# Kernel optimization log

Hardware: AMD Instinct MI355X
Metric: run time of the kernel (lower is better)

Reference implementation:

```python
import jax, jax.numpy as jnp
import numpy as np

TAU = 0.85  # augmented=True -> tau=0.85


def _f1_rewards(labels_f):
    # labels_f: [B, L] binary relevance. Vectorized f1@(k) for k=1..L,
    # replacing the original per-element Python double loop.
    B, L = labels_f.shape
    cum = jnp.cumsum(labels_f, axis=1)                      # rel hits @ k
    k = jnp.arange(1, L + 1, dtype=labels_f.dtype)          # [L]
    prec = cum / k                                          # precision@k
    total = cum[:, -1:]                                     # total relevant per row
    rec = jnp.where(total > 0, cum / jnp.maximum(total, 1.0), 0.0)
    denom = prec + rec
    return jnp.where(denom > 0, 2.0 * prec * rec / jnp.maximum(denom, 1e-30), 0.0)


def setup_inputs() -> dict:
    key = jax.random.key(0)
    k1, k2 = jax.random.split(key)
    B, L = 1024, 4096
    raw = jax.random.uniform(k1, (B, L, 1), dtype=jnp.float32) + 1e-3
    output = raw / jnp.sum(raw, axis=1, keepdims=True)      # valid prob dist per row
    labels = jax.random.randint(k2, (B, L), 0, 2, dtype=jnp.int32)
    return {"output": output, "labels": labels}


def reference(output, labels):
    B = output.shape[0]
    r = _f1_rewards(labels.astype(jnp.float32))             # [B, L]
    q = jax.nn.softmax(r / TAU, axis=1)                     # exp(r/tau)/sum == softmax
    p = output[..., 0]                                      # squeeze(2) -> [B, L]
    logp = jnp.log(p)
    # KLDivLoss(reduction='batchmean'): sum(q * (log q - log p)) / B
    return jnp.sum(q * (jnp.log(q) - logp)) / B
```

## Files before the change

### kernel.cpp

```cpp
#include <hip/hip_runtime.h>


constexpr int L = 4096;

__global__ __launch_bounds__(256) void row_kl_kernel(const float* __restrict__ p,
                                                     const int* __restrict__ labels,
                                                     float* __restrict__ row_out) {
    const int b = blockIdx.x;
    const int t = threadIdx.x;
    const int lane = t & 63;
    const int wv = t >> 6;

    const int4* lab4 = (const int4*)(labels + (size_t)b * L) + t * 4;
    const float4* p4 = (const float4*)(p + (size_t)b * L) + t * 4;

    int4 a0 = lab4[0], a1 = lab4[1], a2 = lab4[2], a3 = lab4[3];
    float4 q0 = p4[0], q1 = p4[1], q2 = p4[2], q3 = p4[3];

    int lv[16] = {a0.x, a0.y, a0.z, a0.w, a1.x, a1.y, a1.z, a1.w,
                  a2.x, a2.y, a2.z, a2.w, a3.x, a3.y, a3.z, a3.w};
    float pv[16] = {q0.x, q0.y, q0.z, q0.w, q1.x, q1.y, q1.z, q1.w,
                    q2.x, q2.y, q2.z, q2.w, q3.x, q3.y, q3.z, q3.w};

    int tsum = 0;
    #pragma unroll
    for (int j = 0; j < 16; ++j) tsum += lv[j];

    int inc = tsum;
    #pragma unroll
    for (int d = 1; d < 64; d <<= 1) {
        int n = __shfl_up(inc, d, 64);
        if (lane >= d) inc += n;
    }

    __shared__ int wsum[4];
    __shared__ float red[8];
    if (lane == 63) wsum[wv] = inc;
    __syncthreads();
    const int w0 = wsum[0], w1 = wsum[1], w2 = wsum[2], w3 = wsum[3];
    const int T = w0 + w1 + w2 + w3;
    int run = (wv > 0 ? w0 : 0) + (wv > 1 ? w1 : 0) + (wv > 2 ? w2 : 0)
              + inc - tsum;

    const float K = 2.0f / 0.85f;
    float Zl = 0.f, Wl = 0.f;
    const int base = t * 16 + 1;
    #pragma unroll
    for (int j = 0; j < 16; ++j) {
        run += lv[j];
        float s = K * __fdividef((float)run, (float)(T + base + j));
        float e = __expf(s);
        Zl += e;
        Wl += e * (s - __logf(pv[j]));
    }

    #pragma unroll
    for (int d = 32; d >= 1; d >>= 1) {
        Zl += __shfl_down(Zl, d, 64);
        Wl += __shfl_down(Wl, d, 64);
    }
    if (lane == 0) { red[wv] = Zl; red[4 + wv] = Wl; }
    __syncthreads();
    if (t == 0) {
        float Z = red[0] + red[1] + red[2] + red[3];
        float W = red[4] + red[5] + red[6] + red[7];
        row_out[b] = W / Z - __logf(Z);
    }
}

__global__ __launch_bounds__(256) void final_reduce_kernel(const float* __restrict__ row,
                                                           float* __restrict__ out, int B) {
    const int t = threadIdx.x;
    float v = 0.f;
    for (int i = t; i < B; i += 256) v += row[i];
    #pragma unroll
    for (int d = 32; d >= 1; d >>= 1) v += __shfl_down(v, d, 64);
    __shared__ float s[4];
    if ((t & 63) == 0) s[t >> 6] = v;
    __syncthreads();
    if (t == 0) out[0] = (s[0] + s[1] + s[2] + s[3]) / (float)B;
}

extern "C" void kernel_launch(void* const* d_in, const int* in_sizes, int n_in,
                              void* d_out, int out_size, void* d_ws, size_t ws_size,
                              hipStream_t stream) {
    const float* p = (const float*)d_in[0];
    const int* labels = (const int*)d_in[1];
    const int B = in_sizes[1] / L;
    float* row = (float*)d_ws;

    row_kl_kernel<<<B, 256, 0, stream>>>(p, labels, row);
    final_reduce_kernel<<<1, 256, 0, stream>>>(row, (float*)d_out, B);
}
```

Baseline: 77.69 us.

## Coalesce row loads by interleaving per-lane chunks and scanning each chunk separately

```diff
diff --git a/kernel.cpp b/kernel.cpp
--- a/kernel.cpp
+++ b/kernel.cpp
@@ -11,47 +11,64 @@
     const int lane = t & 63;
     const int wv = t >> 6;
 
-    const int4* lab4 = (const int4*)(labels + (size_t)b * L) + t * 4;
-    const float4* p4 = (const float4*)(p + (size_t)b * L) + t * 4;
+    const size_t rowoff = (size_t)b * L;
+    const int qbase = wv * 1024;
 
-    int4 a0 = lab4[0], a1 = lab4[1], a2 = lab4[2], a3 = lab4[3];
-    float4 q0 = p4[0], q1 = p4[1], q2 = p4[2], q3 = p4[3];
-
-    int lv[16] = {a0.x, a0.y, a0.z, a0.w, a1.x, a1.y, a1.z, a1.w,
-                  a2.x, a2.y, a2.z, a2.w, a3.x, a3.y, a3.z, a3.w};
-    float pv[16] = {q0.x, q0.y, q0.z, q0.w, q1.x, q1.y, q1.z, q1.w,
-                    q2.x, q2.y, q2.z, q2.w, q3.x, q3.y, q3.z, q3.w};
-
-    int tsum = 0;
+    int4 a[4];
+    float4 q[4];
     #pragma unroll
-    for (int j = 0; j < 16; ++j) tsum += lv[j];
-
-    int inc = tsum;
-    #pragma unroll
-    for (int d = 1; d < 64; d <<= 1) {
-        int n = __shfl_up(inc, d, 64);
-        if (lane >= d) inc += n;
+    for (int c = 0; c < 4; ++c) {
+        const int e0 = qbase + 256 * c + 4 * lane;
+        a[c] = *(const int4*)(labels + rowoff + e0);
+        q[c] = *(const float4*)(p + rowoff + e0);
     }
 
-    __shared__ int wsum[4];
+    int rs[4];
+    #pragma unroll
+    for (int c = 0; c < 4; ++c) rs[c] = a[c].x + a[c].y + a[c].z + a[c].w;
+
+    int inc[4];
+    #pragma unroll
+    for (int c = 0; c < 4; ++c) {
+        int v = rs[c];
+        #pragma unroll
+        for (int d = 1; d < 64; d <<= 1) {
+            int n = __shfl_up(v, d, 64);
+            if (lane >= d) v += n;
+        }
+        inc[c] = v;
+    }
+    int ct[4];
+    #pragma unroll
+    for (int c = 0; c < 4; ++c) ct[c] = __shfl(inc[c], 63, 64);
+
+    const int qt = ct[0] + ct[1] + ct[2] + ct[3];
+    __shared__ int qsum[4];
     __shared__ float red[8];
-    if (lane == 63) wsum[wv] = inc;
+    if (lane == 0) qsum[wv] = qt;
     __syncthreads();
-    const int w0 = wsum[0], w1 = wsum[1], w2 = wsum[2], w3 = wsum[3];
-    const int T = w0 + w1 + w2 + w3;
-    int run = (wv > 0 ? w0 : 0) + (wv > 1 ? w1 : 0) + (wv > 2 ? w2 : 0)
-              + inc - tsum;
+    const int s0 = qsum[0], s1 = qsum[1], s2 = qsum[2], s3 = qsum[3];
+    const int T = s0 + s1 + s2 + s3;
+    const int qpre = (wv > 0 ? s0 : 0) + (wv > 1 ? s1 : 0) + (wv > 2 ? s2 : 0);
 
     const float K = 2.0f / 0.85f;
     float Zl = 0.f, Wl = 0.f;
-    const int base = t * 16 + 1;
     #pragma unroll
-    for (int j = 0; j < 16; ++j) {
-        run += lv[j];
-        float s = K * __fdividef((float)run, (float)(T + base + j));
-        float e = __expf(s);
-        Zl += e;
-        Wl += e * (s - __logf(pv[j]));
+    for (int c = 0; c < 4; ++c) {
+        int run = qpre + (c > 0 ? ct[0] : 0) + (c > 1 ? ct[1] : 0) + (c > 2 ? ct[2] : 0)
+                  + inc[c] - rs[c];
+        float kf = (float)(T + qbase + 256 * c + 4 * lane + 1);
+        const int lv[4] = {a[c].x, a[c].y, a[c].z, a[c].w};
+        const float pv[4] = {q[c].x, q[c].y, q[c].z, q[c].w};
+        #pragma unroll
+        for (int j = 0; j < 4; ++j) {
+            run += lv[j];
+            float s = K * __fdividef((float)run, kf);
+            kf += 1.0f;
+            float e = __expf(s);
+            Zl += e;
+            Wl += e * (s - __logf(pv[j]));
+        }
     }
 
     #pragma unroll
```

Measured after the change: 78.33 us. No clear change (+0.8%).
